# Kernel optimization log

Hardware: AMD Instinct MI355X
Metric: run time of the kernel (lower is better)

Reference implementation:

```python
import jax, jax.numpy as jnp
import numpy as np


def _hard_sigmoid(x):
    # Keras ConvLSTM2D default recurrent_activation
    return jnp.clip(0.2 * x + 0.5, 0.0, 1.0)


def _conv(x, w):
    # NHWC input, HWIO kernel, SAME padding, stride 1
    return jax.lax.conv_general_dilated(
        x, w, (1, 1), 'SAME', dimension_numbers=('NHWC', 'HWIO', 'NHWC'))


def _convlstm(seq, h, c, k, rk, b):
    # seq: [B, T, H, W, Cin]; h, c: [B, H, W, F]
    # k: [kh, kw, Cin, 4F], rk: [kh, kw, F, 4F], b: [4F]
    def step(carry, x):
        h, c = carry
        z = _conv(x, k) + _conv(h, rk) + b  # [B,H,W,4F]
        zi, zf, zc, zo = jnp.split(z, 4, axis=-1)
        i = _hard_sigmoid(zi)
        f = _hard_sigmoid(zf)
        o = _hard_sigmoid(zo)
        c = f * c + i * jnp.tanh(zc)
        h = o * jnp.tanh(c)
        return (h, c), None
    (h, c), _ = jax.lax.scan(step, (h, c), jnp.swapaxes(seq, 0, 1))
    return h, c


def setup_inputs() -> dict:
    key = jax.random.key(0)
    ks = jax.random.split(key, 14)
    B, T, H, W, Cin, F, K = 32, 1, 64, 64, 1, 64, 3
    s = 0.05
    inp = {
        'input_': jax.random.normal(ks[0], (B, T, H, W, Cin), jnp.float32),
        'h0': jax.random.normal(ks[1], (B, H, W, F), jnp.float32) * s,
        'c0': jax.random.normal(ks[2], (B, H, W, F), jnp.float32) * s,
        'h1': jax.random.normal(ks[3], (B, H, W, F), jnp.float32) * s,
        'c1': jax.random.normal(ks[4], (B, H, W, F), jnp.float32) * s,
        'k0': jax.random.normal(ks[5], (K, K, Cin, 4 * F), jnp.float32) * s,
        'rk0': jax.random.normal(ks[6], (K, K, F, 4 * F), jnp.float32) * s,
        'b0': jnp.zeros((4 * F,), jnp.float32),
        'k1': jax.random.normal(ks[7], (K, K, F, 4 * F), jnp.float32) * s,
        'rk1': jax.random.normal(ks[8], (K, K, F, 4 * F), jnp.float32) * s,
        'b1': jnp.zeros((4 * F,), jnp.float32),
        'cw': jax.random.normal(ks[9], (1, 1, F, 1), jnp.float32) * s,
        'cb': jnp.zeros((1,), jnp.float32),
    }
    return inp


def reference(input_, h0, c0, h1, c1, k0, rk0, b0, k1, rk1, b1, cw, cb):
    # Layer 0 consumes the input frame sequence (T=1)
    h0n, c0n = _convlstm(input_, h0, c0, k0, rk0, b0)
    # Layer 1 consumes layer-0's last hidden state as its (length-1) input
    h1n, c1n = _convlstm(h0n[:, None], h1, c1, k1, rk1, b1)
    frames = _conv(h1n, cw) + cb  # 1x1 conv head -> [B,H,W,1]
    return frames, h0n, c0n, h1n, c1n
```

## Files before the change

### kernel.cpp

```cpp
#include <hip/hip_runtime.h>
#include <hip/hip_bf16.h>

typedef short s16;
typedef __attribute__((ext_vector_type(8))) short bf16x8;
typedef __attribute__((ext_vector_type(4))) float f32x4;

__device__ __forceinline__ s16 f2bf(float f) {
  unsigned u = __builtin_bit_cast(unsigned, f);
  unsigned r = (u + 0x7FFFu + ((u >> 16) & 1u)) >> 16;
  return (s16)r;
}

__device__ __forceinline__ float hsig(float x) {
  return fminf(fmaxf(0.2f * x + 0.5f, 0.0f), 1.0f);
}

__global__ void cvt_kernel(const float* __restrict__ src, s16* __restrict__ dst, int n4) {
  int i = blockIdx.x * blockDim.x + threadIdx.x;
  int stride = gridDim.x * blockDim.x;
  for (; i < n4; i += stride) {
    float4 v = reinterpret_cast<const float4*>(src)[i];
    short4 o;
    o.x = f2bf(v.x); o.y = f2bf(v.y); o.z = f2bf(v.z); o.w = f2bf(v.w);
    reinterpret_cast<short4*>(dst)[i] = o;
  }
}

__global__ void wtrans_kernel(const float* __restrict__ rk, s16* __restrict__ wt) {
  int idx = blockIdx.x * blockDim.x + threadIdx.x;
  if (idx >= 9 * 256 * 64) return;
  int ic = idx & 63;
  int oc = (idx >> 6) & 255;
  int tap = idx >> 14;
  wt[idx] = f2bf(rk[(tap * 64 + ic) * 256 + oc]);
}

__global__ void k0trans_kernel(const float* __restrict__ k0, s16* __restrict__ wt) {
  int idx = blockIdx.x * blockDim.x + threadIdx.x;
  if (idx >= 256 * 32) return;
  int kk = idx & 31;
  int oc = idx >> 5;
  wt[idx] = (kk < 9) ? f2bf(k0[kk * 256 + oc]) : (s16)0;
}

#define PXS 66
#define ROWSZ (PXS * 64)
#define SRCSZ (6 * ROWSZ)
template <int NSRC, bool XPATH>
__global__ __launch_bounds__(1024, 4) void cell_kernel(
    const s16* __restrict__ src0,
    const s16* __restrict__ src1,
    const s16* __restrict__ w0,
    const s16* __restrict__ w1,
    const float* __restrict__ xin,
    const s16* __restrict__ k0t,
    const float* __restrict__ bias,
    const float* __restrict__ c_old,
    float* __restrict__ h_out,
    float* __restrict__ c_out,
    s16* __restrict__ hb_out)
{
  __shared__ __align__(16) s16 a_lds[NSRC * SRCSZ];
  __shared__ __align__(16) s16 w_lds[2][8192];
  __shared__ float x_lds[XPATH ? 384 : 1];

  const int tid = threadIdx.x;
  const int b  = blockIdx.x >> 4;
  const int y0 = (blockIdx.x & 15) << 2;

  for (int s = 0; s < NSRC; ++s) {
    const s16* src = (s == 0) ? src0 : src1;
    #pragma unroll
    for (int i = 0; i < 3; ++i) {
      int c   = tid + i * 1024;
      int row = c >> 9;
      int px  = (c >> 3) & 63;
      int cb  = c & 7;
      int y   = y0 - 1 + row;
      bf16x8 val = {};
      if ((unsigned)y < 64u)
        val = *reinterpret_cast<const bf16x8*>(src + (((b * 64 + y) * 64 + px) * 64 + cb * 8));
      int xp  = px + 1;
      *reinterpret_cast<bf16x8*>(a_lds + s * SRCSZ + (row * PXS + xp) * 64 + ((cb ^ (xp & 7)) * 8)) = val;
    }
  }
  if (tid < NSRC * 96) {
    int s   = tid / 96;
    int r   = tid % 96;
    int row = r >> 4;
    int xp  = ((r >> 3) & 1) ? 65 : 0;
    int cb  = r & 7;
    bf16x8 z = {};
    *reinterpret_cast<bf16x8*>(a_lds + s * SRCSZ + (row * PXS + xp) * 64 + cb * 8) = z;
  }
  if (XPATH) {
    if (tid < 384) {
      int row = tid >> 6, px = tid & 63;
      int y = y0 - 1 + row;
      x_lds[tid] = ((unsigned)y < 64u) ? xin[(b * 64 + y) * 64 + px] : 0.0f;
    }
  }
  __syncthreads();

  const int wave = tid >> 6;
  const int lane = tid & 63;
  const int g    = wave & 3;
  const int mh   = wave >> 2;
  const int l15  = lane & 15;
  const int l4   = lane >> 4;

  f32x4 acc[4][4] = {};

  const int w_goff = (tid & 255) * 64 + (tid >> 8) * 8;
  char* wl0 = (char*)(&w_lds[0][0]) + ((tid >> 6) << 10);
  auto issueW = [&](int u) {
    int t2 = u >> 1, k = u & 1;
    int si  = (NSRC == 2 && t2 >= 9) ? 1 : 0;
    int tap = t2 - 9 * si;
    const s16* wt = (si ? w1 : w0) + tap * 16384 + k * 32 + w_goff;
    char* dst = wl0 + ((u & 1) ? 16384 : 0);
    __builtin_amdgcn_global_load_lds((const __attribute__((address_space(1))) void*)wt,
                                     (__attribute__((address_space(3))) void*)dst, 16, 0, 0);
  };

  if (XPATH) {
    bf16x8 bx[4];
    #pragma unroll
    for (int j = 0; j < 4; ++j) {
      int oc = j * 64 + g * 16 + l15;
      bx[j] = *reinterpret_cast<const bf16x8*>(k0t + oc * 32 + l4 * 8);
    }
    #pragma unroll
    for (int m = 0; m < 4; ++m) {
      int px = m * 16 + l15;
      bf16x8 ax = {};
      #pragma unroll
      for (int j = 0; j < 8; ++j) {
        int t = l4 * 8 + j;
        if (t < 9) {
          int dy = t / 3, dx = t - dy * 3;
          int xx = px + dx - 1;
          float xv = ((unsigned)xx < 64u) ? x_lds[(mh + dy) * 64 + xx] : 0.0f;
          ax[j] = f2bf(xv);
        }
      }
      #pragma unroll
      for (int j = 0; j < 4; ++j)
        acc[m][j] = __builtin_amdgcn_mfma_f32_16x16x32_bf16(ax, bx[j], acc[m][j], 0, 0, 0);
    }
  }

  constexpr int NST = NSRC * 18;
  issueW(0);
  #pragma unroll
  for (int u = 0; u < NST; ++u) {
    issueW((u + 1 == NST) ? 0 : u + 1);
    asm volatile("s_waitcnt vmcnt(1)" ::: "memory");
    __builtin_amdgcn_s_barrier();
    __builtin_amdgcn_sched_barrier(0);

    const char* wb = (const char*)(&w_lds[u & 1][0]);
    bf16x8 wf[4];
    #pragma unroll
    for (int j = 0; j < 4; ++j) {
      int oc = j * 64 + g * 16 + l15;
      wf[j] = *reinterpret_cast<const bf16x8*>(wb + l4 * 4096 + oc * 16);
    }
    int t2 = u >> 1, k = u & 1;
    int si  = (NSRC == 2 && t2 >= 9) ? 1 : 0;
    int tap = t2 - 9 * si;
    int dy = tap / 3, dx = tap - dy * 3;
    const char* lb = (const char*)a_lds + si * (SRCSZ * 2) + (mh + dy) * (ROWSZ * 2);
    #pragma unroll
    for (int m = 0; m < 4; ++m) {
      int xq   = m * 16 + l15 + dx;
      int boff = xq * 128 + (((k << 6) | (l4 << 4)) ^ ((xq & 7) << 4));
      bf16x8 a = *reinterpret_cast<const bf16x8*>(lb + boff);
      #pragma unroll
      for (int j = 0; j < 4; ++j)
        acc[m][j] = __builtin_amdgcn_mfma_f32_16x16x32_bf16(a, wf[j], acc[m][j], 0, 0, 0);
    }
    __builtin_amdgcn_sched_barrier(0);
    __builtin_amdgcn_s_barrier();
  }

  float bi[4];
  #pragma unroll
  for (int j = 0; j < 4; ++j) bi[j] = bias[j * 64 + g * 16 + l15];

  const int pix_base = b * 4096 + y0 * 64;
  const int f = g * 16 + l15;
  #pragma unroll
  for (int m = 0; m < 4; ++m) {
    #pragma unroll
    for (int r = 0; r < 4; ++r) {
      int pl = mh * 64 + m * 16 + l4 * 4 + r;
      int off = (pix_base + pl) * 64 + f;
      float zi = acc[m][0][r] + bi[0];
      float zf = acc[m][1][r] + bi[1];
      float zc = acc[m][2][r] + bi[2];
      float zo = acc[m][3][r] + bi[3];
      float ig = hsig(zi), fg = hsig(zf), og = hsig(zo);
      float cn = fg * c_old[off] + ig * tanhf(zc);
      float hn = og * tanhf(cn);
      c_out[off] = cn;
      h_out[off] = hn;
      if (hb_out) hb_out[off] = f2bf(hn);
    }
  }
}

__global__ void frames_kernel(const float* __restrict__ h, const float* __restrict__ cw,
                              const float* __restrict__ cbp, float* __restrict__ out) {
  int tid = blockIdx.x * 256 + threadIdx.x;
  int p  = tid >> 2;
  int fc = (tid & 3) * 16;
  const float4* hp = reinterpret_cast<const float4*>(h + p * 64 + fc);
  const float4* wp = reinterpret_cast<const float4*>(cw + fc);
  float s = 0.0f;
  #pragma unroll
  for (int i = 0; i < 4; ++i) {
    float4 v = hp[i];
    float4 w = wp[i];
    s += v.x * w.x + v.y * w.y + v.z * w.z + v.w * w.w;
  }
  s += __shfl_xor(s, 1);
  s += __shfl_xor(s, 2);
  if ((tid & 3) == 0) out[p] = s + cbp[0];
}

extern "C" void kernel_launch(void* const* d_in, const int* in_sizes, int n_in,
                              void* d_out, int out_size, void* d_ws, size_t ws_size,
                              hipStream_t stream) {
  const float* x   = (const float*)d_in[0];
  const float* h0  = (const float*)d_in[1];
  const float* c0  = (const float*)d_in[2];
  const float* h1  = (const float*)d_in[3];
  const float* c1  = (const float*)d_in[4];
  const float* k0  = (const float*)d_in[5];
  const float* rk0 = (const float*)d_in[6];
  const float* b0  = (const float*)d_in[7];
  const float* k1  = (const float*)d_in[8];
  const float* rk1 = (const float*)d_in[9];
  const float* b1  = (const float*)d_in[10];
  const float* cw  = (const float*)d_in[11];
  const float* cbp = (const float*)d_in[12];

  float* out    = (float*)d_out;
  float* frames = out;
  float* h0n    = out + 131072;
  float* c0n    = out + 131072 + 8388608;
  float* h1n    = out + 131072 + 2 * 8388608;
  float* c1n    = out + 131072 + 3 * 8388608;

  char* ws = (char*)d_ws;
  const size_t SZ_H = 16777216;
  s16* h0b  = (s16*)(ws + 0 * SZ_H);
  s16* h1b  = (s16*)(ws + 1 * SZ_H);
  s16* h0nb = (s16*)(ws + 2 * SZ_H);
  s16* w0t  = (s16*)(ws + 3 * SZ_H);
  s16* w1t  = (s16*)(ws + 3 * SZ_H + 1 * 294912);
  s16* w2t  = (s16*)(ws + 3 * SZ_H + 2 * 294912);
  s16* k0t  = (s16*)(ws + 3 * SZ_H + 3 * 294912);

  cvt_kernel<<<2048, 256, 0, stream>>>(h0, h0b, 2097152);
  cvt_kernel<<<2048, 256, 0, stream>>>(h1, h1b, 2097152);
  wtrans_kernel<<<576, 256, 0, stream>>>(rk0, w0t);
  wtrans_kernel<<<576, 256, 0, stream>>>(k1, w1t);
  wtrans_kernel<<<576, 256, 0, stream>>>(rk1, w2t);
  k0trans_kernel<<<32, 256, 0, stream>>>(k0, k0t);

  cell_kernel<1, true><<<512, 1024, 0, stream>>>(
      h0b, nullptr, w0t, nullptr, x, k0t, b0, c0, h0n, c0n, h0nb);

  cell_kernel<2, false><<<512, 1024, 0, stream>>>(
      h0nb, h1b, w1t, w2t, nullptr, nullptr, b1, c1, h1n, c1n, nullptr);

  frames_kernel<<<2048, 256, 0, stream>>>(h1n, cw, cbp, frames);
}
```

Measured before the change: 219.5 us.

## Fuse hidden-state bf16 conversion into cell kernels and triple-buffer weight loads

Removes the separate fp32-to-bf16 conversion kernels for h0 and h1: the cell kernels now read fp32 directly and convert while staging into LDS. The four weight-prep kernels are merged into one launch. The weight pipeline moves to a three-slot ring with register double-buffering, so the next stage's fragments are read before the current MFMAs and one barrier per stage is dropped. This cuts launches and a round trip through HBM for the bf16 copies, at the cost of more LDS, more registers and doubled fp32 read traffic in the staging phase.

```diff
diff --git a/kernel.cpp b/kernel.cpp
--- a/kernel.cpp
+++ b/kernel.cpp
@@ -15,41 +15,51 @@
   return fminf(fmaxf(0.2f * x + 0.5f, 0.0f), 1.0f);
 }
 
-__global__ void cvt_kernel(const float* __restrict__ src, s16* __restrict__ dst, int n4) {
-  int i = blockIdx.x * blockDim.x + threadIdx.x;
-  int stride = gridDim.x * blockDim.x;
-  for (; i < n4; i += stride) {
-    float4 v = reinterpret_cast<const float4*>(src)[i];
-    short4 o;
-    o.x = f2bf(v.x); o.y = f2bf(v.y); o.z = f2bf(v.z); o.w = f2bf(v.w);
-    reinterpret_cast<short4*>(dst)[i] = o;
-  }
-}
-
-__global__ void wtrans_kernel(const float* __restrict__ rk, s16* __restrict__ wt) {
-  int idx = blockIdx.x * blockDim.x + threadIdx.x;
-  if (idx >= 9 * 256 * 64) return;
-  int ic = idx & 63;
-  int oc = (idx >> 6) & 255;
-  int tap = idx >> 14;
-  wt[idx] = f2bf(rk[(tap * 64 + ic) * 256 + oc]);
-}
-
-__global__ void k0trans_kernel(const float* __restrict__ k0, s16* __restrict__ wt) {
-  int idx = blockIdx.x * blockDim.x + threadIdx.x;
-  if (idx >= 256 * 32) return;
-  int kk = idx & 31;
-  int oc = idx >> 5;
-  wt[idx] = (kk < 9) ? f2bf(k0[kk * 256 + oc]) : (s16)0;
+__global__ void wprep_kernel(const float* __restrict__ rk0, const float* __restrict__ k1,
+                             const float* __restrict__ rk1, const float* __restrict__ k0,
+                             s16* __restrict__ w0t, s16* __restrict__ w1t,
+                             s16* __restrict__ w2t, s16* __restrict__ k0t) {
+  int idx = blockIdx.x * 256 + threadIdx.x;
+  const int n1 = 9 * 256 * 64;
+  if (idx < 3 * n1) {
+    int which = idx / n1;
+    int r = idx - which * n1;
+    int ic = r & 63;
+    int oc = (r >> 6) & 255;
+    int tap = r >> 14;
+    const float* src = (which == 0) ? rk0 : (which == 1) ? k1 : rk1;
+    s16* dst = (which == 0) ? w0t : (which == 1) ? w1t : w2t;
+    dst[r] = f2bf(src[(tap * 64 + ic) * 256 + oc]);
+  } else if (idx < 3 * n1 + 8192) {
+    int r = idx - 3 * n1;
+    int kk = r & 31;
+    int oc = r >> 5;
+    k0t[r] = (kk < 9) ? f2bf(k0[kk * 256 + oc]) : (s16)0;
+  }
 }
 
 #define PXS 66
 #define ROWSZ (PXS * 64)
 #define SRCSZ (6 * ROWSZ)
-template <int NSRC, bool XPATH>
+template <bool F32>
+__device__ __forceinline__ bf16x8 load_conv8(const void* src, long off) {
+  if constexpr (F32) {
+    const float* p = (const float*)src + off;
+    float4 v0 = *reinterpret_cast<const float4*>(p);
+    float4 v1 = *reinterpret_cast<const float4*>(p + 4);
+    bf16x8 r;
+    r[0] = f2bf(v0.x); r[1] = f2bf(v0.y); r[2] = f2bf(v0.z); r[3] = f2bf(v0.w);
+    r[4] = f2bf(v1.x); r[5] = f2bf(v1.y); r[6] = f2bf(v1.z); r[7] = f2bf(v1.w);
+    return r;
+  } else {
+    return *reinterpret_cast<const bf16x8*>((const s16*)src + off);
+  }
+}
+
+template <int NSRC, bool XPATH, bool S0F32, bool S1F32>
 __global__ __launch_bounds__(1024, 4) void cell_kernel(
-    const s16* __restrict__ src0,
-    const s16* __restrict__ src1,
+    const void* __restrict__ src0,
+    const void* __restrict__ src1,
     const s16* __restrict__ w0,
     const s16* __restrict__ w1,
     const float* __restrict__ xin,
@@ -61,27 +71,30 @@
     s16* __restrict__ hb_out)
 {
   __shared__ __align__(16) s16 a_lds[NSRC * SRCSZ];
-  __shared__ __align__(16) s16 w_lds[2][8192];
+  __shared__ __align__(16) s16 w_lds[3][8192];
   __shared__ float x_lds[XPATH ? 384 : 1];
 
   const int tid = threadIdx.x;
   const int b  = blockIdx.x >> 4;
   const int y0 = (blockIdx.x & 15) << 2;
 
-  for (int s = 0; s < NSRC; ++s) {
-    const s16* src = (s == 0) ? src0 : src1;
-    #pragma unroll
-    for (int i = 0; i < 3; ++i) {
-      int c   = tid + i * 1024;
-      int row = c >> 9;
-      int px  = (c >> 3) & 63;
-      int cb  = c & 7;
-      int y   = y0 - 1 + row;
-      bf16x8 val = {};
-      if ((unsigned)y < 64u)
-        val = *reinterpret_cast<const bf16x8*>(src + (((b * 64 + y) * 64 + px) * 64 + cb * 8));
-      int xp  = px + 1;
-      *reinterpret_cast<bf16x8*>(a_lds + s * SRCSZ + (row * PXS + xp) * 64 + ((cb ^ (xp & 7)) * 8)) = val;
+  #pragma unroll
+  for (int i = 0; i < 3; ++i) {
+    int c   = tid + i * 1024;
+    int row = c >> 9;
+    int px  = (c >> 3) & 63;
+    int cb  = c & 7;
+    int y   = y0 - 1 + row;
+    int xp  = px + 1;
+    long goff = ((long)(b * 64 + y) * 64 + px) * 64 + cb * 8;
+    int  doff = (row * PXS + xp) * 64 + ((cb ^ (xp & 7)) * 8);
+    bf16x8 v0 = {};
+    if ((unsigned)y < 64u) v0 = load_conv8<S0F32>(src0, goff);
+    *reinterpret_cast<bf16x8*>(a_lds + doff) = v0;
+    if (NSRC == 2) {
+      bf16x8 v1 = {};
+      if ((unsigned)y < 64u) v1 = load_conv8<S1F32>(src1, goff);
+      *reinterpret_cast<bf16x8*>(a_lds + SRCSZ + doff) = v1;
     }
   }
   if (tid < NSRC * 96) {
@@ -100,7 +113,6 @@
       x_lds[tid] = ((unsigned)y < 64u) ? xin[(b * 64 + y) * 64 + px] : 0.0f;
     }
   }
-  __syncthreads();
 
   const int wave = tid >> 6;
   const int lane = tid & 63;
@@ -109,19 +121,25 @@
   const int l15  = lane & 15;
   const int l4   = lane >> 4;
 
-  f32x4 acc[4][4] = {};
-
+  constexpr int NST = NSRC * 18;
   const int w_goff = (tid & 255) * 64 + (tid >> 8) * 8;
   char* wl0 = (char*)(&w_lds[0][0]) + ((tid >> 6) << 10);
   auto issueW = [&](int u) {
-    int t2 = u >> 1, k = u & 1;
+    int uu = (u >= NST) ? u - NST : u;
+    int t2 = uu >> 1, k = uu & 1;
     int si  = (NSRC == 2 && t2 >= 9) ? 1 : 0;
     int tap = t2 - 9 * si;
     const s16* wt = (si ? w1 : w0) + tap * 16384 + k * 32 + w_goff;
-    char* dst = wl0 + ((u & 1) ? 16384 : 0);
+    char* dst = wl0 + (uu % 3) * 16384;
     __builtin_amdgcn_global_load_lds((const __attribute__((address_space(1))) void*)wt,
                                      (__attribute__((address_space(3))) void*)dst, 16, 0, 0);
   };
+
+  issueW(0);
+  issueW(1);
+  __syncthreads();
+
+  f32x4 acc[4][4] = {};
 
   if (XPATH) {
     bf16x8 bx[4];
@@ -150,22 +168,17 @@
     }
   }
 
-  constexpr int NST = NSRC * 18;
-  issueW(0);
-  #pragma unroll
-  for (int u = 0; u < NST; ++u) {
-    issueW((u + 1 == NST) ? 0 : u + 1);
-    asm volatile("s_waitcnt vmcnt(1)" ::: "memory");
-    __builtin_amdgcn_s_barrier();
-    __builtin_amdgcn_sched_barrier(0);
-
-    const char* wb = (const char*)(&w_lds[u & 1][0]);
-    bf16x8 wf[4];
+  const char* wbuf  = (const char*)(&w_lds[0][0]);
+  const int   wroff = l4 * 4096;
+  auto readW = [&](bf16x8* wf, int slot) {
+    const char* wb = wbuf + slot * 16384 + wroff;
     #pragma unroll
     for (int j = 0; j < 4; ++j) {
       int oc = j * 64 + g * 16 + l15;
-      wf[j] = *reinterpret_cast<const bf16x8*>(wb + l4 * 4096 + oc * 16);
-    }
+      wf[j] = *reinterpret_cast<const bf16x8*>(wb + oc * 16);
+    }
+  };
+  auto doStage = [&](const bf16x8* wf, int u) {
     int t2 = u >> 1, k = u & 1;
     int si  = (NSRC == 2 && t2 >= 9) ? 1 : 0;
     int tap = t2 - 9 * si;
@@ -180,7 +193,21 @@
       for (int j = 0; j < 4; ++j)
         acc[m][j] = __builtin_amdgcn_mfma_f32_16x16x32_bf16(a, wf[j], acc[m][j], 0, 0, 0);
     }
-    __builtin_amdgcn_sched_barrier(0);
+  };
+
+  bf16x8 wfA[4], wfB[4];
+  readW(wfA, 0);
+  #pragma unroll
+  for (int u = 0; u < NST; u += 2) {
+    issueW(u + 2);
+    readW(wfB, (u + 1) % 3);
+    doStage(wfA, u);
+    asm volatile("s_waitcnt vmcnt(0)" ::: "memory");
+    __builtin_amdgcn_s_barrier();
+    issueW(u + 3);
+    readW(wfA, (u + 2) % 3);
+    doStage(wfB, u + 1);
+    asm volatile("s_waitcnt vmcnt(0)" ::: "memory");
     __builtin_amdgcn_s_barrier();
   }
 
@@ -255,26 +282,19 @@
 
   char* ws = (char*)d_ws;
   const size_t SZ_H = 16777216;
-  s16* h0b  = (s16*)(ws + 0 * SZ_H);
-  s16* h1b  = (s16*)(ws + 1 * SZ_H);
-  s16* h0nb = (s16*)(ws + 2 * SZ_H);
-  s16* w0t  = (s16*)(ws + 3 * SZ_H);
-  s16* w1t  = (s16*)(ws + 3 * SZ_H + 1 * 294912);
-  s16* w2t  = (s16*)(ws + 3 * SZ_H + 2 * 294912);
-  s16* k0t  = (s16*)(ws + 3 * SZ_H + 3 * 294912);
-
-  cvt_kernel<<<2048, 256, 0, stream>>>(h0, h0b, 2097152);
-  cvt_kernel<<<2048, 256, 0, stream>>>(h1, h1b, 2097152);
-  wtrans_kernel<<<576, 256, 0, stream>>>(rk0, w0t);
-  wtrans_kernel<<<576, 256, 0, stream>>>(k1, w1t);
-  wtrans_kernel<<<576, 256, 0, stream>>>(rk1, w2t);
-  k0trans_kernel<<<32, 256, 0, stream>>>(k0, k0t);
-
-  cell_kernel<1, true><<<512, 1024, 0, stream>>>(
-      h0b, nullptr, w0t, nullptr, x, k0t, b0, c0, h0n, c0n, h0nb);
-
-  cell_kernel<2, false><<<512, 1024, 0, stream>>>(
-      h0nb, h1b, w1t, w2t, nullptr, nullptr, b1, c1, h1n, c1n, nullptr);
+  s16* h0nb = (s16*)(ws + 0 * SZ_H);
+  s16* w0t  = (s16*)(ws + 1 * SZ_H);
+  s16* w1t  = (s16*)(ws + 1 * SZ_H + 1 * 294912);
+  s16* w2t  = (s16*)(ws + 1 * SZ_H + 2 * 294912);
+  s16* k0t  = (s16*)(ws + 1 * SZ_H + 3 * 294912);
+
+  wprep_kernel<<<1760, 256, 0, stream>>>(rk0, k1, rk1, k0, w0t, w1t, w2t, k0t);
+
+  cell_kernel<1, true, true, false><<<512, 1024, 0, stream>>>(
+      h0, nullptr, w0t, nullptr, x, k0t, b0, c0, h0n, c0n, h0nb);
+
+  cell_kernel<2, false, false, true><<<512, 1024, 0, stream>>>(
+      h0nb, h1, w1t, w2t, nullptr, nullptr, b1, c1, h1n, c1n, nullptr);
 
   frames_kernel<<<2048, 256, 0, stream>>>(h1n, cw, cbp, frames);
 }
```

Result: faster. 209.0 us (-4.8%).
